# Performance work log

Hardware: AMD Instinct MI355X
Metric: run time of the kernel (lower is better)

Reference implementation:

```python
import jax, jax.numpy as jnp
import numpy as np

BS, M, D_IN, D_OUT = 32, 128, 64, 32


def _spd_log(X):
    # torch.svd on an SPD matrix == eigh (u diag(s) u^T with s>0), so
    # u @ diag(log s) @ v^T reduces to u @ diag(log s) @ u^T.
    s, u = jnp.linalg.eigh(X)
    return jnp.einsum('...ik,...k,...jk->...ij', u, jnp.log(s), u)


def _sym_exp(X):
    s, u = jnp.linalg.eigh(X)
    return jnp.einsum('...ik,...k,...jk->...ij', u, jnp.exp(s), u)


def setup_inputs() -> dict:
    key = jax.random.key(0)
    kx, kq, kk, kv = jax.random.split(key, 4)
    A = jax.random.normal(kx, (BS, M, D_IN, D_IN), dtype=jnp.float32)
    # SPD input: A A^T / d_in + eps I (eigenvalues strictly positive)
    x = jnp.einsum('bmij,bmkj->bmik', A, A) / D_IN + 1e-2 * jnp.eye(D_IN, dtype=jnp.float32)
    def stiefel(k):
        # column-orthonormal (d_in, d_out), mimicking SPDTransform's Stiefel weight
        return jnp.linalg.qr(jax.random.normal(k, (D_IN, D_OUT), dtype=jnp.float32))[0]
    return {'x': x, 'Wq': stiefel(kq), 'Wk': stiefel(kk), 'Wv': stiefel(kv)}


def reference(x, Wq, Wk, Wv):
    bs, m, d_in, _ = x.shape
    d_out = Wq.shape[1]

    def bimap(W):  # SPDTransform: W^T X W, stays SPD
        return jnp.einsum('pi,bmpq,qj->bmij', W, x, W)

    Q, K, V = bimap(Wq), bimap(Wk), bimap(Wv)
    logQ, logK, logV = _spd_log(Q), _spd_log(K), _spd_log(V)

    # log-Euclidean distance: sum of singular values of D D^T with
    # D = log A - log B (symmetric) equals trace(D D^T) = ||D||_F^2.
    # Torch's repeat/expand pattern yields energy[b,i,j] = d(K_i, Q_j);
    # computed here without materializing the (bs, m, m, d, d) tensor.
    q2 = jnp.sum(logQ * logQ, axis=(-2, -1))            # [bs, m]
    k2 = jnp.sum(logK * logK, axis=(-2, -1))            # [bs, m]
    cross = jnp.einsum('bikl,bjkl->bij', logK, logQ)    # [bs, m(i=K), m(j=Q)]
    energy = k2[:, :, None] + q2[:, None, :] - 2.0 * cross

    scores = 1.0 / (1.0 + jnp.log1p(energy))
    # softmax over dim=-2 (the K index i), then permute(0, 2, 1)
    attn = jnp.swapaxes(jax.nn.softmax(scores, axis=-2), -1, -2)  # [bs, j, i]

    # LogEuclideanMean: exp_sym( sum_i attn[b,j,i] * log V[b,i] )
    mean_log = jnp.einsum('bji,bikl->bjkl', attn, logV)
    out = _sym_exp(mean_log)
    return out.reshape(bs * m, d_out, d_out)
```

## Files before the change

kernel.cpp:

```cpp
#include <hip/hip_runtime.h>
#include <math.h>

constexpr int kBS = 32, kM = 128, kNMAT = kBS * kM;
constexpr int kDIN = 64, kDOUT = 32, kMSZ = kDOUT * kDOUT;
constexpr int kNSweep = 5;

constexpr size_t OFF_SS   = (size_t)3 * kNMAT * kMSZ;
constexpr size_t OFF_ATTN = OFF_SS + (size_t)3 * kNMAT;

#define F4(p)  (*(float4*)(p))
#define CF4(p) (*(const float4*)(p))

__global__ __launch_bounds__(256) void k_bimap(
    const float* __restrict__ x, const float* __restrict__ Wq,
    const float* __restrict__ Wk, const float* __restrict__ Wv,
    float* __restrict__ P) {
  __shared__ float Xs[64 * 68];
  __shared__ float Wsh[64 * 32];
  __shared__ float Ts[64 * 36];
  const int t = threadIdx.x;
  const int bm = blockIdx.x;
  const float* xp = x + (size_t)bm * (kDIN * kDIN);
  {
    const int f0 = t * 16;
    const int r = f0 >> 6, c = f0 & 63;
    const float* src = xp + f0;
    float* dst = &Xs[r * 68 + c];
#pragma unroll
    for (int i = 0; i < 4; ++i) F4(dst + 4 * i) = CF4(src + 4 * i);
  }
  const int r0 = (t >> 3) * 2;
  const int j0 = (t & 7) * 4;
  const int i2 = t >> 3;
  for (int tt = 0; tt < 3; ++tt) {
    const float* W = (tt == 0) ? Wq : ((tt == 1) ? Wk : Wv);
    __syncthreads();
    F4(&Wsh[t * 8]) = CF4(W + t * 8);
    F4(&Wsh[t * 8 + 4]) = CF4(W + t * 8 + 4);
    __syncthreads();
    float a0[4] = {0.f, 0.f, 0.f, 0.f}, a1[4] = {0.f, 0.f, 0.f, 0.f};
    for (int k = 0; k < 64; ++k) {
      const float x0 = Xs[r0 * 68 + k];
      const float x1 = Xs[(r0 + 1) * 68 + k];
      const float4 w = CF4(&Wsh[k * 32 + j0]);
      a0[0] += x0 * w.x; a0[1] += x0 * w.y; a0[2] += x0 * w.z; a0[3] += x0 * w.w;
      a1[0] += x1 * w.x; a1[1] += x1 * w.y; a1[2] += x1 * w.z; a1[3] += x1 * w.w;
    }
    F4(&Ts[r0 * 36 + j0])       = make_float4(a0[0], a0[1], a0[2], a0[3]);
    F4(&Ts[(r0 + 1) * 36 + j0]) = make_float4(a1[0], a1[1], a1[2], a1[3]);
    __syncthreads();
    float b4[4] = {0.f, 0.f, 0.f, 0.f};
    for (int p = 0; p < 64; ++p) {
      const float wv = Wsh[p * 32 + i2];
      const float4 tv = CF4(&Ts[p * 36 + j0]);
      b4[0] += wv * tv.x; b4[1] += wv * tv.y; b4[2] += wv * tv.z; b4[3] += wv * tv.w;
    }
    F4(&P[((size_t)tt * kNMAT + bm) * kMSZ + i2 * 32 + j0]) =
        make_float4(b4[0], b4[1], b4[2], b4[3]);
  }
}

constexpr int kJSlot = 32 * 36 + 32;
constexpr int kShl1 = 0x101, kShr1 = 0x111;

template <int CTRL>
__device__ __forceinline__ float updppf(float old_, float x) {
  return __builtin_bit_cast(float,
      __builtin_amdgcn_update_dpp(__builtin_bit_cast(int, old_),
                                  __builtin_bit_cast(int, x),
                                  CTRL, 0xf, 0xf, false));
}

__device__ __forceinline__ float xsign(float x, float s) {
  return __builtin_bit_cast(float,
      __builtin_bit_cast(int, x) ^
      (__builtin_bit_cast(int, s) & 0x80000000));
}

__global__ __launch_bounds__(256, 4) void k_jacobi_log(float* __restrict__ P,
                                                       float* __restrict__ sq) {
  __shared__ float lds[8 * kJSlot];
  const int t = threadIdx.x;
  const int wid = t >> 6, lane = t & 63;
  const int g = lane & 15;
  const int sub = (lane >> 4) & 1;
  const int off = sub * 16;
  const size_t gid = (size_t)blockIdx.x * 8 + wid * 2 + (lane >> 5);
  float* A = P + gid * kMSZ;

  const bool is_g0 = (g == 0);
  const int p0 = is_g0 ? 31 : g;
  const int q0 = is_g0 ? 0 : 31 - g;

  float cp[16], cq[16];
  {
    const float* pr = A + p0 * 32 + off;
    const float* qr = A + q0 * 32 + off;
#pragma unroll
    for (int i = 0; i < 16; i += 4) {
      const float4 a = CF4(pr + i);
      cp[i] = a.x; cp[i + 1] = a.y; cp[i + 2] = a.z; cp[i + 3] = a.w;
      const float4 b = CF4(qr + i);
      cq[i] = b.x; cq[i + 1] = b.y; cq[i + 2] = b.z; cq[i + 3] = b.w;
    }
  }
  float app = 0.f, aqq = 0.f;
#pragma unroll
  for (int i = 0; i < 16; ++i) {
    app = fmaf(cp[i], cp[i], app);
    aqq = fmaf(cq[i], cq[i], aqq);
  }
  app += __shfl_xor(app, 16);
  aqq += __shfl_xor(aqq, 16);

  for (int sw = 0; sw < kNSweep; ++sw) {
    for (int r = 0; r < 31; ++r) {
      float d0 = cp[0] * cq[0], d1 = cp[1] * cq[1];
#pragma unroll
      for (int i = 2; i < 16; i += 2) {
        d0 = fmaf(cp[i], cq[i], d0);
        d1 = fmaf(cp[i + 1], cq[i + 1], d1);
      }
      float apq = d0 + d1;
      apq += __shfl_xor(apq, 16);
      const float d = aqq - app;
      const float apq2 = 2.f * apq;
      float h2 = fmaf(d, d, apq2 * apq2);
      h2 = fmaxf(h2, 1e-38f);
      const float hr = __builtin_amdgcn_rsqf(h2);
      const float h = h2 * hr;
      const float den = fabsf(d) + h;
      const float t0 = apq2 * __builtin_amdgcn_rcpf(den);
      const float tt = xsign(t0, d);
      const float c = __builtin_amdgcn_rsqf(fmaf(tt, tt, 1.f));
      const float sn = tt * c;
      float np[16], nq[16];
#pragma unroll
      for (int i = 0; i < 16; ++i) {
        const float t1 = c * cp[i];
        const float t2 = sn * cp[i];
        np[i] = fmaf(-sn, cq[i], t1);
        nq[i] = fmaf(c, cq[i], t2);
      }
      const float c2 = c * c, s2 = sn * sn, cs2 = 2.f * c * sn;
      const float capp = fmaf(c2, app, fmaf(s2, aqq, -cs2 * apq));
      const float caqq = (app + aqq) - capp;
#pragma unroll
      for (int i = 0; i < 16; ++i) {
        const float cpm = updppf<kShl1>(nq[i], np[i]);
        cp[i] = is_g0 ? np[i] : cpm;
        cq[i] = updppf<kShr1>(cpm, nq[i]);
      }
      {
        const float capm = updppf<kShl1>(caqq, capp);
        app = is_g0 ? capp : capm;
        aqq = updppf<kShr1>(capm, caqq);
      }
    }
  }
  {
    float* Bs = lds + (wid * 2 + (lane >> 5)) * kJSlot;
#pragma unroll
    for (int i = 0; i < 16; i += 4) {
      F4(&Bs[p0 * 36 + off + i]) = make_float4(cp[i], cp[i+1], cp[i+2], cp[i+3]);
      F4(&Bs[q0 * 36 + off + i]) = make_float4(cq[i], cq[i+1], cq[i+2], cq[i+3]);
    }
  }
  __builtin_amdgcn_wave_barrier();
  const size_t gbase = (size_t)blockIdx.x * 8 + wid * 2;
#pragma unroll
  for (int m = 0; m < 2; ++m) {
    float* Bs = lds + (wid * 2 + m) * kJSlot;
    float* ncol = Bs + 1152;
    const size_t gm = gbase + m;
    float* Am = P + gm * kMSZ;
    {
      const int cc_ = lane & 31, h = lane >> 5;
      const float* col = &Bs[cc_ * 36 + h * 16];
      float ssum = 0.f;
#pragma unroll
      for (int i = 0; i < 16; i += 4) {
        const float4 v = CF4(col + i);
        ssum += v.x * v.x + v.y * v.y + v.z * v.z + v.w * v.w;
      }
      ssum += __shfl_xor(ssum, 32);
      const float lg = 0.5f * logf(ssum);
      float tot = lg * lg;
      tot += __shfl_xor(tot, 1);  tot += __shfl_xor(tot, 2);
      tot += __shfl_xor(tot, 4);  tot += __shfl_xor(tot, 8);
      tot += __shfl_xor(tot, 16); tot += __shfl_xor(tot, 32);
      if (lane == 0) sq[gm] = 0.5f * tot;
      if (h == 0) ncol[cc_] = lg / ssum;
    }
    __builtin_amdgcn_wave_barrier();
    {
      const int rr = (lane >> 3) * 4, cc = (lane & 7) * 4;
      float acc[4][4] = {};
      for (int c = 0; c < 32; ++c) {
        const float w = ncol[c];
        const float4 br = CF4(&Bs[c * 36 + rr]);
        const float4 bc = CF4(&Bs[c * 36 + cc]);
        const float wr[4]  = {w * br.x, w * br.y, w * br.z, w * br.w};
        const float bcv[4] = {bc.x, bc.y, bc.z, bc.w};
#pragma unroll
        for (int i = 0; i < 4; ++i)
#pragma unroll
          for (int j2 = 0; j2 < 4; ++j2) acc[i][j2] += wr[i] * bcv[j2];
      }
#pragma unroll
      for (int i = 0; i < 4; ++i)
        F4(&Am[(rr + i) * 32 + cc]) =
            make_float4(acc[i][0], acc[i][1], acc[i][2], acc[i][3]);
    }
    __builtin_amdgcn_wave_barrier();
  }
}

__global__ __launch_bounds__(256) void k_attn(
    const float* __restrict__ P, const float* __restrict__ sq,
    float* __restrict__ attn) {
  __shared__ float Ks[128 * 36];
  __shared__ float Qs[32 * 36];
  __shared__ float red[8 * 36];
  __shared__ float mcol[32];
  __shared__ float scol[32];
  const int t = threadIdx.x;
  const int b = blockIdx.y, jt = blockIdx.x;
  const int j0g = jt * 32;
  const float* logK = P + ((size_t)kNMAT + (size_t)b * kM) * kMSZ;
  const float* logQ = P + ((size_t)b * kM + j0g) * kMSZ;
  const int i0 = (t >> 3) * 4, j0 = (t & 7) * 4;
  float acc[4][4] = {};
  for (int dc = 0; dc < kMSZ; dc += 32) {
    __syncthreads();
    {
      const int r = t >> 1, c0 = (t & 1) * 16;
      const float* src = logK + (size_t)r * kMSZ + dc + c0;
      float* dst = &Ks[r * 36 + c0];
#pragma unroll
      for (int i = 0; i < 4; ++i) F4(dst + 4 * i) = CF4(src + 4 * i);
    }
    {
      const int r = t >> 3, c0 = (t & 7) * 4;
      F4(&Qs[r * 36 + c0]) = CF4(logQ + (size_t)r * kMSZ + dc + c0);
    }
    __syncthreads();
    for (int k = 0; k < 32; ++k) {
      float kv[4], qv[4];
#pragma unroll
      for (int i = 0; i < 4; ++i) kv[i] = Ks[(i0 + i) * 36 + k];
#pragma unroll
      for (int j2 = 0; j2 < 4; ++j2) qv[j2] = Qs[(j0 + j2) * 36 + k];
#pragma unroll
      for (int i = 0; i < 4; ++i)
#pragma unroll
        for (int j2 = 0; j2 < 4; ++j2) acc[i][j2] += kv[i] * qv[j2];
    }
  }
  __syncthreads();
  {
    float k2v[4], q2v[4];
#pragma unroll
    for (int i = 0; i < 4; ++i) k2v[i] = sq[kNMAT + b * kM + i0 + i];
#pragma unroll
    for (int j2 = 0; j2 < 4; ++j2) q2v[j2] = sq[b * kM + j0g + j0 + j2];
#pragma unroll
    for (int i = 0; i < 4; ++i)
#pragma unroll
      for (int j2 = 0; j2 < 4; ++j2) {
        float e = k2v[i] + q2v[j2] - 2.f * acc[i][j2];
        e = fmaxf(e, 0.f);
        Ks[(i0 + i) * 36 + (j0 + j2)] = 1.f / (1.f + log1pf(e));
      }
  }
  __syncthreads();
  const int jl = t & 31, grp = t >> 5;
  {
    float m = -1e30f;
    for (int i = grp * 16; i < grp * 16 + 16; ++i) m = fmaxf(m, Ks[i * 36 + jl]);
    red[grp * 36 + jl] = m;
  }
  __syncthreads();
  if (t < 32) {
    float m = red[t];
#pragma unroll
    for (int g = 1; g < 8; ++g) m = fmaxf(m, red[g * 36 + t]);
    mcol[t] = m;
  }
  __syncthreads();
  {
    const float mj = mcol[jl];
    float s = 0.f;
    for (int i = grp * 16; i < grp * 16 + 16; ++i) s += expf(Ks[i * 36 + jl] - mj);
    red[grp * 36 + jl] = s;
  }
  __syncthreads();
  if (t < 32) {
    float s = red[t];
#pragma unroll
    for (int g = 1; g < 8; ++g) s += red[g * 36 + t];
    scol[t] = 1.f / s;
  }
  __syncthreads();
  {
    const int il = t & 31, jg = t >> 5;
#pragma unroll
    for (int rep = 0; rep < 4; ++rep) {
      const int j2 = jg + rep * 8;
      const float mj = mcol[j2], is = scol[j2];
      float* dst = attn + ((size_t)b * kM + j0g + j2) * kM;
#pragma unroll
      for (int c4 = 0; c4 < 4; ++c4) {
        const int i = il + c4 * 32;
        dst[i] = expf(Ks[i * 36 + j2] - mj) * is;
      }
    }
  }
}

__global__ __launch_bounds__(256) void k_meanlog(
    const float* __restrict__ attn, const float* __restrict__ P,
    float* __restrict__ ML) {
  __shared__ float As[32 * 132];
  __shared__ float Vs[128 * 64];
  const int t = threadIdx.x;
  const int b = blockIdx.y, jt = blockIdx.x;
  const int j0g = jt * 32;
  const float* logV = P + ((size_t)2 * kNMAT + (size_t)b * kM) * kMSZ;
  {
    const int r = t >> 3, c0 = (t & 7) * 16;
    const float* src = attn + ((size_t)b * kM + j0g + r) * kM + c0;
    float* dst = &As[r * 132 + c0];
#pragma unroll
    for (int i = 0; i < 4; ++i) F4(dst + 4 * i) = CF4(src + 4 * i);
  }
  const int j0 = (t >> 4) * 2, d0 = (t & 15) * 4;
  for (int dc = 0; dc < kMSZ; dc += 64) {
    __syncthreads();
    {
      const int r = t >> 1, c0 = (t & 1) * 32;
      const float* src = logV + (size_t)r * kMSZ + dc + c0;
      float* dst = &Vs[r * 64 + c0];
#pragma unroll
      for (int i = 0; i < 8; ++i) F4(dst + 4 * i) = CF4(src + 4 * i);
    }
    __syncthreads();
    float a0[4] = {0.f,0.f,0.f,0.f}, a1[4] = {0.f,0.f,0.f,0.f};
    for (int k = 0; k < kM; ++k) {
      const float w0 = As[(j0 + 0) * 132 + k];
      const float w1 = As[(j0 + 1) * 132 + k];
      const float4 v = CF4(&Vs[k * 64 + d0]);
      a0[0] += w0 * v.x; a0[1] += w0 * v.y; a0[2] += w0 * v.z; a0[3] += w0 * v.w;
      a1[0] += w1 * v.x; a1[1] += w1 * v.y; a1[2] += w1 * v.z; a1[3] += w1 * v.w;
    }
    F4(&ML[((size_t)b * kM + j0g + j0 + 0) * kMSZ + dc + d0]) =
        make_float4(a0[0], a0[1], a0[2], a0[3]);
    F4(&ML[((size_t)b * kM + j0g + j0 + 1) * kMSZ + dc + d0]) =
        make_float4(a1[0], a1[1], a1[2], a1[3]);
  }
}

constexpr int kESlot = 2 * 1152;

__global__ __launch_bounds__(256) void k_expm(const float* __restrict__ ML,
                                              float* __restrict__ out) {
  __shared__ float lds[4 * kESlot];
  const int t = threadIdx.x;
  const int wid = t >> 6, lane = t & 63;
  const size_t bm = (size_t)blockIdx.x * 4 + wid;
  float* Mb = lds + wid * kESlot;
  float* Tb = Mb + 1152;
  const float* S = ML + bm * kMSZ;
  const int r = lane >> 1, c0 = (lane & 1) * 16;
  float4 v0 = CF4(S + r * 32 + c0),     v1 = CF4(S + r * 32 + c0 + 4),
         v2 = CF4(S + r * 32 + c0 + 8), v3 = CF4(S + r * 32 + c0 + 12);
  float lsum = v0.x*v0.x + v0.y*v0.y + v0.z*v0.z + v0.w*v0.w
             + v1.x*v1.x + v1.y*v1.y + v1.z*v1.z + v1.w*v1.w
             + v2.x*v2.x + v2.y*v2.y + v2.z*v2.z + v2.w*v2.w
             + v3.x*v3.x + v3.y*v3.y + v3.z*v3.z + v3.w*v3.w;
#pragma unroll
  for (int d = 1; d < 64; d <<= 1) lsum += __shfl_xor(lsum, d);
  const float fn = sqrtf(lsum);
  int sc = 0;
  if (fn > 0.5f) sc = (int)ceilf(log2f(fn * 2.0f));
  const float scale = exp2f((float)(-sc));
  v0.x*=scale; v0.y*=scale; v0.z*=scale; v0.w*=scale;
  v1.x*=scale; v1.y*=scale; v1.z*=scale; v1.w*=scale;
  v2.x*=scale; v2.y*=scale; v2.z*=scale; v2.w*=scale;
  v3.x*=scale; v3.y*=scale; v3.z*=scale; v3.w*=scale;
  F4(&Mb[r * 36 + c0])      = v0;
  F4(&Mb[r * 36 + c0 + 4])  = v1;
  F4(&Mb[r * 36 + c0 + 8])  = v2;
  F4(&Mb[r * 36 + c0 + 12]) = v3;
  __builtin_amdgcn_wave_barrier();
  const int rr = (lane >> 3) * 4, cc = (lane & 7) * 4;
#pragma unroll
  for (int i = 0; i < 4; ++i) {
    float4 v = F4(&Mb[(rr + i) * 36 + cc]);
    v.x = v.x * 0.1f + ((rr + i == cc + 0) ? 1.f : 0.f);
    v.y = v.y * 0.1f + ((rr + i == cc + 1) ? 1.f : 0.f);
    v.z = v.z * 0.1f + ((rr + i == cc + 2) ? 1.f : 0.f);
    v.w = v.w * 0.1f + ((rr + i == cc + 3) ? 1.f : 0.f);
    F4(&Tb[(rr + i) * 36 + cc]) = v;
  }
  __builtin_amdgcn_wave_barrier();
  for (int j = 9; j >= 1; --j) {
    float a4[4][4] = {};
    for (int k = 0; k < 32; ++k) {
      float mv[4];
#pragma unroll
      for (int i = 0; i < 4; ++i) mv[i] = Mb[(rr + i) * 36 + k];
      const float4 tv = CF4(&Tb[k * 36 + cc]);
      const float tvv[4] = {tv.x, tv.y, tv.z, tv.w};
#pragma unroll
      for (int i = 0; i < 4; ++i)
#pragma unroll
        for (int j2 = 0; j2 < 4; ++j2) a4[i][j2] += mv[i] * tvv[j2];
    }
    const float inv = 1.f / (float)j;
#pragma unroll
    for (int i = 0; i < 4; ++i) {
      float4 v;
      v.x = a4[i][0] * inv + ((rr + i == cc + 0) ? 1.f : 0.f);
      v.y = a4[i][1] * inv + ((rr + i == cc + 1) ? 1.f : 0.f);
      v.z = a4[i][2] * inv + ((rr + i == cc + 2) ? 1.f : 0.f);
      v.w = a4[i][3] * inv + ((rr + i == cc + 3) ? 1.f : 0.f);
      F4(&Tb[(rr + i) * 36 + cc]) = v;
    }
    __builtin_amdgcn_wave_barrier();
  }
  for (int st = 0; st < sc; ++st) {
    float a4[4][4] = {};
    for (int k = 0; k < 32; ++k) {
      float mv[4];
#pragma unroll
      for (int i = 0; i < 4; ++i) mv[i] = Tb[(rr + i) * 36 + k];
      const float4 tv = CF4(&Tb[k * 36 + cc]);
      const float tvv[4] = {tv.x, tv.y, tv.z, tv.w};
#pragma unroll
      for (int i = 0; i < 4; ++i)
#pragma unroll
        for (int j2 = 0; j2 < 4; ++j2) a4[i][j2] += mv[i] * tvv[j2];
    }
#pragma unroll
    for (int i = 0; i < 4; ++i)
      F4(&Tb[(rr + i) * 36 + cc]) =
          make_float4(a4[i][0], a4[i][1], a4[i][2], a4[i][3]);
    __builtin_amdgcn_wave_barrier();
  }
#pragma unroll
  for (int i = 0; i < 4; ++i) {
    const float4 v = CF4(&Tb[(rr + i) * 36 + cc]);
    F4(&out[bm * kMSZ + (rr + i) * 32 + cc]) = v;
  }
}

extern "C" void kernel_launch(void* const* d_in, const int* in_sizes, int n_in,
                              void* d_out, int out_size, void* d_ws, size_t ws_size,
                              hipStream_t stream) {
  const float* x  = (const float*)d_in[0];
  const float* Wq = (const float*)d_in[1];
  const float* Wk = (const float*)d_in[2];
  const float* Wv = (const float*)d_in[3];
  float* ws   = (float*)d_ws;
  float* P    = ws;
  float* sq   = ws + OFF_SS;
  float* attn = ws + OFF_ATTN;
  float* ML   = ws;
  float* out  = (float*)d_out;

  k_bimap<<<kNMAT, 256, 0, stream>>>(x, Wq, Wk, Wv, P);
  k_jacobi_log<<<3 * kNMAT / 8, 256, 0, stream>>>(P, sq);
  k_attn<<<dim3(4, kBS), 256, 0, stream>>>(P, sq, attn);
  k_meanlog<<<dim3(4, kBS), 256, 0, stream>>>(attn, P, ML);
  k_expm<<<kNMAT / 4, 256, 0, stream>>>(ML, out);
}
```

Before: 501.7 us.

## Cut Jacobi sweeps, retile attention and mean-log, use symmetry for vector LDS reads

Result: faster. 420.4 us (-16.2%).

```diff
diff --git a/kernel.cpp b/kernel.cpp
--- a/kernel.cpp
+++ b/kernel.cpp
@@ -3,7 +3,7 @@
 
 constexpr int kBS = 32, kM = 128, kNMAT = kBS * kM;
 constexpr int kDIN = 64, kDOUT = 32, kMSZ = kDOUT * kDOUT;
-constexpr int kNSweep = 5;
+constexpr int kNSweep = 4;
 
 constexpr size_t OFF_SS   = (size_t)3 * kNMAT * kMSZ;
 constexpr size_t OFF_ATTN = OFF_SS + (size_t)3 * kNMAT;
@@ -40,11 +40,10 @@
     __syncthreads();
     float a0[4] = {0.f, 0.f, 0.f, 0.f}, a1[4] = {0.f, 0.f, 0.f, 0.f};
     for (int k = 0; k < 64; ++k) {
-      const float x0 = Xs[r0 * 68 + k];
-      const float x1 = Xs[(r0 + 1) * 68 + k];
+      const float2 x01 = *(const float2*)&Xs[k * 68 + r0];
       const float4 w = CF4(&Wsh[k * 32 + j0]);
-      a0[0] += x0 * w.x; a0[1] += x0 * w.y; a0[2] += x0 * w.z; a0[3] += x0 * w.w;
-      a1[0] += x1 * w.x; a1[1] += x1 * w.y; a1[2] += x1 * w.z; a1[3] += x1 * w.w;
+      a0[0] += x01.x * w.x; a0[1] += x01.x * w.y; a0[2] += x01.x * w.z; a0[3] += x01.x * w.w;
+      a1[0] += x01.y * w.x; a1[1] += x01.y * w.y; a1[2] += x01.y * w.z; a1[3] += x01.y * w.w;
     }
     F4(&Ts[r0 * 36 + j0])       = make_float4(a0[0], a0[1], a0[2], a0[3]);
     F4(&Ts[(r0 + 1) * 36 + j0]) = make_float4(a1[0], a1[1], a1[2], a1[3]);
@@ -219,100 +218,110 @@
 __global__ __launch_bounds__(256) void k_attn(
     const float* __restrict__ P, const float* __restrict__ sq,
     float* __restrict__ attn) {
-  __shared__ float Ks[128 * 36];
-  __shared__ float Qs[32 * 36];
-  __shared__ float red[8 * 36];
-  __shared__ float mcol[32];
-  __shared__ float scol[32];
+  __shared__ float Kt[32 * 132];
+  __shared__ float Qt[32 * 20];
+  __shared__ float Ss[128 * 20];
+  __shared__ float red[16 * 20];
+  __shared__ float mcol[16];
+  __shared__ float scol[16];
   const int t = threadIdx.x;
   const int b = blockIdx.y, jt = blockIdx.x;
-  const int j0g = jt * 32;
+  const int j0g = jt * 16;
   const float* logK = P + ((size_t)kNMAT + (size_t)b * kM) * kMSZ;
   const float* logQ = P + ((size_t)b * kM + j0g) * kMSZ;
-  const int i0 = (t >> 3) * 4, j0 = (t & 7) * 4;
-  float acc[4][4] = {};
+  const int i0 = (t >> 3) * 4, j0 = (t & 7) * 2;
+  float acc[4][2] = {};
   for (int dc = 0; dc < kMSZ; dc += 32) {
     __syncthreads();
     {
       const int r = t >> 1, c0 = (t & 1) * 16;
       const float* src = logK + (size_t)r * kMSZ + dc + c0;
-      float* dst = &Ks[r * 36 + c0];
-#pragma unroll
-      for (int i = 0; i < 4; ++i) F4(dst + 4 * i) = CF4(src + 4 * i);
+#pragma unroll
+      for (int ii = 0; ii < 16; ii += 4) {
+        const float4 v = CF4(src + ii);
+        Kt[(c0 + ii + 0) * 132 + r] = v.x;
+        Kt[(c0 + ii + 1) * 132 + r] = v.y;
+        Kt[(c0 + ii + 2) * 132 + r] = v.z;
+        Kt[(c0 + ii + 3) * 132 + r] = v.w;
+      }
     }
     {
-      const int r = t >> 3, c0 = (t & 7) * 4;
-      F4(&Qs[r * 36 + c0]) = CF4(logQ + (size_t)r * kMSZ + dc + c0);
+      const int j = t >> 4, c0 = (t & 15) * 2;
+      const float2 v = *(const float2*)(logQ + (size_t)j * kMSZ + dc + c0);
+      Qt[(c0 + 0) * 20 + j] = v.x;
+      Qt[(c0 + 1) * 20 + j] = v.y;
     }
     __syncthreads();
     for (int k = 0; k < 32; ++k) {
-      float kv[4], qv[4];
-#pragma unroll
-      for (int i = 0; i < 4; ++i) kv[i] = Ks[(i0 + i) * 36 + k];
-#pragma unroll
-      for (int j2 = 0; j2 < 4; ++j2) qv[j2] = Qs[(j0 + j2) * 36 + k];
-#pragma unroll
-      for (int i = 0; i < 4; ++i)
-#pragma unroll
-        for (int j2 = 0; j2 < 4; ++j2) acc[i][j2] += kv[i] * qv[j2];
-    }
-  }
-  __syncthreads();
-  {
-    float k2v[4], q2v[4];
+      const float4 kv = CF4(&Kt[k * 132 + i0]);
+      const float2 qv = *(const float2*)&Qt[k * 20 + j0];
+      acc[0][0] = fmaf(kv.x, qv.x, acc[0][0]);
+      acc[0][1] = fmaf(kv.x, qv.y, acc[0][1]);
+      acc[1][0] = fmaf(kv.y, qv.x, acc[1][0]);
+      acc[1][1] = fmaf(kv.y, qv.y, acc[1][1]);
+      acc[2][0] = fmaf(kv.z, qv.x, acc[2][0]);
+      acc[2][1] = fmaf(kv.z, qv.y, acc[2][1]);
+      acc[3][0] = fmaf(kv.w, qv.x, acc[3][0]);
+      acc[3][1] = fmaf(kv.w, qv.y, acc[3][1]);
+    }
+  }
+  {
+    float k2v[4], q2v[2];
 #pragma unroll
     for (int i = 0; i < 4; ++i) k2v[i] = sq[kNMAT + b * kM + i0 + i];
 #pragma unroll
-    for (int j2 = 0; j2 < 4; ++j2) q2v[j2] = sq[b * kM + j0g + j0 + j2];
+    for (int j2 = 0; j2 < 2; ++j2) q2v[j2] = sq[b * kM + j0g + j0 + j2];
 #pragma unroll
     for (int i = 0; i < 4; ++i)
 #pragma unroll
-      for (int j2 = 0; j2 < 4; ++j2) {
+      for (int j2 = 0; j2 < 2; ++j2) {
         float e = k2v[i] + q2v[j2] - 2.f * acc[i][j2];
         e = fmaxf(e, 0.f);
-        Ks[(i0 + i) * 36 + (j0 + j2)] = 1.f / (1.f + log1pf(e));
-      }
-  }
-  __syncthreads();
-  const int jl = t & 31, grp = t >> 5;
+        Ss[(i0 + i) * 20 + (j0 + j2)] = 1.f / (1.f + log1pf(e));
+      }
+  }
+  __syncthreads();
+  const int jl = t & 15, grp = t >> 4;
   {
     float m = -1e30f;
-    for (int i = grp * 16; i < grp * 16 + 16; ++i) m = fmaxf(m, Ks[i * 36 + jl]);
-    red[grp * 36 + jl] = m;
-  }
-  __syncthreads();
-  if (t < 32) {
+#pragma unroll
+    for (int i = 0; i < 8; ++i) m = fmaxf(m, Ss[(grp * 8 + i) * 20 + jl]);
+    red[grp * 20 + jl] = m;
+  }
+  __syncthreads();
+  if (t < 16) {
     float m = red[t];
 #pragma unroll
-    for (int g = 1; g < 8; ++g) m = fmaxf(m, red[g * 36 + t]);
+    for (int g = 1; g < 16; ++g) m = fmaxf(m, red[g * 20 + t]);
     mcol[t] = m;
   }
   __syncthreads();
   {
     const float mj = mcol[jl];
     float s = 0.f;
-    for (int i = grp * 16; i < grp * 16 + 16; ++i) s += expf(Ks[i * 36 + jl] - mj);
-    red[grp * 36 + jl] = s;
-  }
-  __syncthreads();
-  if (t < 32) {
+#pragma unroll
+    for (int i = 0; i < 8; ++i) s += expf(Ss[(grp * 8 + i) * 20 + jl] - mj);
+    red[grp * 20 + jl] = s;
+  }
+  __syncthreads();
+  if (t < 16) {
     float s = red[t];
 #pragma unroll
-    for (int g = 1; g < 8; ++g) s += red[g * 36 + t];
+    for (int g = 1; g < 16; ++g) s += red[g * 20 + t];
     scol[t] = 1.f / s;
   }
   __syncthreads();
   {
     const int il = t & 31, jg = t >> 5;
 #pragma unroll
-    for (int rep = 0; rep < 4; ++rep) {
+    for (int rep = 0; rep < 2; ++rep) {
       const int j2 = jg + rep * 8;
       const float mj = mcol[j2], is = scol[j2];
       float* dst = attn + ((size_t)b * kM + j0g + j2) * kM;
 #pragma unroll
       for (int c4 = 0; c4 < 4; ++c4) {
         const int i = il + c4 * 32;
-        dst[i] = expf(Ks[i * 36 + j2] - mj) * is;
+        dst[i] = expf(Ss[i * 20 + j2] - mj) * is;
       }
     }
   }
@@ -321,43 +330,42 @@
 __global__ __launch_bounds__(256) void k_meanlog(
     const float* __restrict__ attn, const float* __restrict__ P,
     float* __restrict__ ML) {
-  __shared__ float As[32 * 132];
-  __shared__ float Vs[128 * 64];
+  __shared__ float As[16 * 132];
   const int t = threadIdx.x;
   const int b = blockIdx.y, jt = blockIdx.x;
-  const int j0g = jt * 32;
+  const int j0g = jt * 16;
   const float* logV = P + ((size_t)2 * kNMAT + (size_t)b * kM) * kMSZ;
   {
-    const int r = t >> 3, c0 = (t & 7) * 16;
-    const float* src = attn + ((size_t)b * kM + j0g + r) * kM + c0;
-    float* dst = &As[r * 132 + c0];
-#pragma unroll
-    for (int i = 0; i < 4; ++i) F4(dst + 4 * i) = CF4(src + 4 * i);
-  }
-  const int j0 = (t >> 4) * 2, d0 = (t & 15) * 4;
-  for (int dc = 0; dc < kMSZ; dc += 64) {
-    __syncthreads();
-    {
-      const int r = t >> 1, c0 = (t & 1) * 32;
-      const float* src = logV + (size_t)r * kMSZ + dc + c0;
-      float* dst = &Vs[r * 64 + c0];
-#pragma unroll
-      for (int i = 0; i < 8; ++i) F4(dst + 4 * i) = CF4(src + 4 * i);
-    }
-    __syncthreads();
-    float a0[4] = {0.f,0.f,0.f,0.f}, a1[4] = {0.f,0.f,0.f,0.f};
-    for (int k = 0; k < kM; ++k) {
-      const float w0 = As[(j0 + 0) * 132 + k];
-      const float w1 = As[(j0 + 1) * 132 + k];
-      const float4 v = CF4(&Vs[k * 64 + d0]);
-      a0[0] += w0 * v.x; a0[1] += w0 * v.y; a0[2] += w0 * v.z; a0[3] += w0 * v.w;
-      a1[0] += w1 * v.x; a1[1] += w1 * v.y; a1[2] += w1 * v.z; a1[3] += w1 * v.w;
-    }
-    F4(&ML[((size_t)b * kM + j0g + j0 + 0) * kMSZ + dc + d0]) =
-        make_float4(a0[0], a0[1], a0[2], a0[3]);
-    F4(&ML[((size_t)b * kM + j0g + j0 + 1) * kMSZ + dc + d0]) =
-        make_float4(a1[0], a1[1], a1[2], a1[3]);
-  }
+    const int j = t >> 4, k0 = (t & 15) * 8;
+    const float* src = attn + ((size_t)b * kM + j0g + j) * kM + k0;
+    F4(&As[j * 132 + k0])     = CF4(src);
+    F4(&As[j * 132 + k0 + 4]) = CF4(src + 4);
+  }
+  __syncthreads();
+  const int d0 = t * 4;
+  float acc[16][4] = {};
+  for (int k = 0; k < kM; k += 4) {
+    float4 vr[4];
+#pragma unroll
+    for (int kk = 0; kk < 4; ++kk)
+      vr[kk] = CF4(&logV[(size_t)(k + kk) * kMSZ + d0]);
+#pragma unroll
+    for (int j = 0; j < 16; ++j) {
+      const float4 w = CF4(&As[j * 132 + k]);
+      const float wv[4] = {w.x, w.y, w.z, w.w};
+#pragma unroll
+      for (int kk = 0; kk < 4; ++kk) {
+        const float* vv = (const float*)&vr[kk];
+#pragma unroll
+        for (int dd = 0; dd < 4; ++dd)
+          acc[j][dd] = fmaf(wv[kk], vv[dd], acc[j][dd]);
+      }
+    }
+  }
+#pragma unroll
+  for (int j = 0; j < 16; ++j)
+    F4(&ML[((size_t)b * kM + j0g + j) * kMSZ + d0]) =
+        make_float4(acc[j][0], acc[j][1], acc[j][2], acc[j][3]);
 }
 
 constexpr int kESlot = 2 * 1152;
@@ -407,15 +415,14 @@
   for (int j = 9; j >= 1; --j) {
     float a4[4][4] = {};
     for (int k = 0; k < 32; ++k) {
-      float mv[4];
-#pragma unroll
-      for (int i = 0; i < 4; ++i) mv[i] = Mb[(rr + i) * 36 + k];
+      const float4 mv = CF4(&Mb[k * 36 + rr]);
+      const float mvv[4] = {mv.x, mv.y, mv.z, mv.w};
       const float4 tv = CF4(&Tb[k * 36 + cc]);
       const float tvv[4] = {tv.x, tv.y, tv.z, tv.w};
 #pragma unroll
       for (int i = 0; i < 4; ++i)
 #pragma unroll
-        for (int j2 = 0; j2 < 4; ++j2) a4[i][j2] += mv[i] * tvv[j2];
+        for (int j2 = 0; j2 < 4; ++j2) a4[i][j2] += mvv[i] * tvv[j2];
     }
     const float inv = 1.f / (float)j;
 #pragma unroll
@@ -432,15 +439,14 @@
   for (int st = 0; st < sc; ++st) {
     float a4[4][4] = {};
     for (int k = 0; k < 32; ++k) {
-      float mv[4];
-#pragma unroll
-      for (int i = 0; i < 4; ++i) mv[i] = Tb[(rr + i) * 36 + k];
+      const float4 mv = CF4(&Tb[k * 36 + rr]);
+      const float mvv[4] = {mv.x, mv.y, mv.z, mv.w};
       const float4 tv = CF4(&Tb[k * 36 + cc]);
       const float tvv[4] = {tv.x, tv.y, tv.z, tv.w};
 #pragma unroll
       for (int i = 0; i < 4; ++i)
 #pragma unroll
-        for (int j2 = 0; j2 < 4; ++j2) a4[i][j2] += mv[i] * tvv[j2];
+        for (int j2 = 0; j2 < 4; ++j2) a4[i][j2] += mvv[i] * tvv[j2];
     }
 #pragma unroll
     for (int i = 0; i < 4; ++i)
@@ -471,7 +477,7 @@
 
   k_bimap<<<kNMAT, 256, 0, stream>>>(x, Wq, Wk, Wv, P);
   k_jacobi_log<<<3 * kNMAT / 8, 256, 0, stream>>>(P, sq);
-  k_attn<<<dim3(4, kBS), 256, 0, stream>>>(P, sq, attn);
-  k_meanlog<<<dim3(4, kBS), 256, 0, stream>>>(attn, P, ML);
+  k_attn<<<dim3(8, kBS), 256, 0, stream>>>(P, sq, attn);
+  k_meanlog<<<dim3(8, kBS), 256, 0, stream>>>(attn, P, ML);
   k_expm<<<kNMAT / 4, 256, 0, stream>>>(ML, out);
 }
```
